# Kernel tuning notes

Hardware: AMD Instinct MI355X
Metric: run time of the kernel (lower is better)

The kernel has to match this reference:

```python
import jax, jax.numpy as jnp
import numpy as np

HEADS = 4
SIZE = 3


def setup_inputs() -> dict:
    key = jax.random.key(0)
    ks = jax.random.split(key, 8)
    B, C, D, H, W = 2, 64, 24, 24, 24
    s = 1.0 / np.sqrt(C)
    x = jax.random.normal(ks[0], (B, C, D, H, W), jnp.float32)
    cemb = jax.random.normal(ks[1], (B, C), jnp.float32)
    Wq = jax.random.normal(ks[2], (C, C), jnp.float32) * s
    bq = jax.random.normal(ks[3], (C,), jnp.float32) * 0.01
    Wk = jax.random.normal(ks[4], (C, C), jnp.float32) * s
    bk = jax.random.normal(ks[5], (C,), jnp.float32) * 0.01
    Wv = jax.random.normal(ks[6], (C, C), jnp.float32) * s
    bv = jax.random.normal(ks[7], (C,), jnp.float32) * 0.01
    return {"x": x, "cemb": cemb, "Wq": Wq, "bq": bq, "Wk": Wk, "bk": bk, "Wv": Wv, "bv": bv}


def _unfold(t, size, heads):
    # t: (B, D, H, W, C) -> (B, D*H*W, heads, size^3, C//heads), zero padded borders
    B, D, H, W, C = t.shape
    pad = size // 2
    tp = jnp.pad(t, ((0, 0), (pad, pad), (pad, pad), (pad, pad), (0, 0)))
    # depth shift outermost, then height, then width (matches torch unfold order)
    patches = jnp.stack(
        [tp[:, i:i + D, j:j + H, l:l + W, :]
         for i in range(size) for j in range(size) for l in range(size)],
        axis=4)  # (B, D, H, W, ws, C)
    ws = size ** 3
    hd = C // heads
    return patches.reshape(B, D * H * W, ws, heads, hd).transpose(0, 1, 3, 2, 4)


def reference(x, cemb, Wq, bq, Wk, bk, Wv, bv):
    # x: (B, C, D, H, W); cemb unused by the original forward
    B, C, D, H, W = x.shape
    heads, size = HEADS, SIZE
    hd = C // heads
    xc = jnp.transpose(x, (0, 2, 3, 4, 1))  # (B, D, H, W, C)
    q = xc @ Wq.T + bq
    k = xc @ Wk.T + bk
    v = xc @ Wv.T + bv
    kw = _unfold(k, size, heads)  # (B, N, h, ws, hd)
    vw = _unfold(v, size, heads)
    qh = q.reshape(B, D * H * W, heads, 1, hd) * (hd ** -0.5)
    attn = jnp.einsum('bnhqd,bnhkd->bnhqk', qh, kw)  # (B, N, h, 1, ws)
    attn = jax.nn.softmax(attn, axis=-1)
    h = jnp.einsum('bnhqk,bnhkd->bnhqd', attn, vw).reshape(B, D, H, W, C)
    out = xc + h
    return jnp.transpose(out, (0, 4, 1, 2, 3))
```

## Files before the change

kernel.cpp:

```cpp
#include <hip/hip_runtime.h>

#define NV 13824
#define CCH 64
#define NB 2

__global__ __launch_bounds__(256) void qkv_kernel(
    const float* __restrict__ x,
    const float* __restrict__ Wq, const float* __restrict__ bq,
    const float* __restrict__ Wk, const float* __restrict__ bk,
    const float* __restrict__ Wv, const float* __restrict__ bv,
    float* __restrict__ qo, float* __restrict__ ko, float* __restrict__ vo)
{
    __shared__ float  sW[32 * 64];
    __shared__ float  sB2[32];
    __shared__ float4 sO[32 * 65];

    const int t   = threadIdx.x;
    const int bid = blockIdx.x;
    const int lb  = (bid & 7) * 81 + (bid >> 3);
    const int oc  = lb % 6;
    const int nch = lb / 6;
    const int m   = oc >> 1;
    const int ch0 = (oc & 1) * 32;
    const int b   = nch / 54;
    const int nn  = (nch - b * 54) * 256;
    const float sc = (m == 0) ? 0.25f : 1.0f;

    {
        const float* const Ws[3] = {Wq, Wk, Wv};
        const float* const bs[3] = {bq, bk, bv};
        const float4* src = (const float4*)(Ws[m] + ch0 * 64);
        float4* dst = (float4*)sW;
        #pragma unroll
        for (int g = 0; g < 2; ++g) {
            float4 wv4 = src[g * 256 + t];
            wv4.x *= sc; wv4.y *= sc; wv4.z *= sc; wv4.w *= sc;
            dst[g * 256 + t] = wv4;
        }
        if (t < 32) sB2[t] = bs[m][ch0 + t] * sc;
    }
    __syncthreads();

    const int tn = t & 63;
    const int tw = t >> 6;
    const float* xp = x + (size_t)b * CCH * NV + nn + tn * 4;
    const float4* sW4 = (const float4*)sW;

    float4 acc[8];
    #pragma unroll
    for (int i = 0; i < 8; ++i) acc[i] = make_float4(0.f, 0.f, 0.f, 0.f);

    #pragma unroll 4
    for (int c4 = 0; c4 < 16; ++c4) {
        float4 w4[8];
        #pragma unroll
        for (int i = 0; i < 8; ++i) w4[i] = sW4[(tw * 8 + i) * 16 + c4];
        #pragma unroll
        for (int cc = 0; cc < 4; ++cc) {
            const float4 xv = *(const float4*)(xp + (size_t)(c4 * 4 + cc) * NV);
            #pragma unroll
            for (int i = 0; i < 8; ++i) {
                const float ws = (cc == 0) ? w4[i].x : (cc == 1) ? w4[i].y
                               : (cc == 2) ? w4[i].z : w4[i].w;
                acc[i].x += xv.x * ws; acc[i].y += xv.y * ws;
                acc[i].z += xv.z * ws; acc[i].w += xv.w * ws;
            }
        }
    }

    #pragma unroll
    for (int i = 0; i < 8; ++i) {
        const int ol = tw * 8 + i;
        const float bb = sB2[ol];
        float4 a = acc[i];
        a.x += bb; a.y += bb; a.z += bb; a.w += bb;
        sO[ol * 65 + tn] = a;
    }
    __syncthreads();

    float* const outs[3] = {qo, ko, vo};
    const float* sOf = (const float*)sO;
    float* ob = outs[m] + (size_t)(b * NV + nn) * 64 + ch0;
    #pragma unroll
    for (int it = 0; it < 8; ++it) {
        const int g   = it * 256 + t;
        const int n   = g >> 3;
        const int of4 = g & 7;
        float4 o4;
        o4.x = sOf[(of4 * 4 + 0) * 260 + n];
        o4.y = sOf[(of4 * 4 + 1) * 260 + n];
        o4.z = sOf[(of4 * 4 + 2) * 260 + n];
        o4.w = sOf[(of4 * 4 + 3) * 260 + n];
        *(float4*)(ob + (size_t)n * 64 + of4 * 4) = o4;
    }
}

__global__ __launch_bounds__(256) void attn_kernel(
    const float* __restrict__ x,
    const float* __restrict__ qw,
    const float* __restrict__ kw,
    const float* __restrict__ vw,
    float* __restrict__ out)
{
    __shared__ float so[32][65];

    const int t    = threadIdx.x;
    const int bid  = blockIdx.x;
    const int lb   = (bid & 7) * 108 + (bid >> 3);
    const int half = t & 1;
    const int head = (t >> 1) & 3;
    const int vb   = t >> 3;
    const int n0g  = lb * 32;
    const int gr   = n0g + vb;
    const int b    = gr / NV;
    const int n    = gr - b * NV;
    const int d    = n / 576;
    const int rem  = n - d * 576;
    const int r    = rem / 24;
    const int w    = rem - r * 24;
    const int coff = head * 16 + half * 8;

    int   idx[27];
    float msk[27];
    #pragma unroll
    for (int i3 = 0; i3 < 3; ++i3)
    #pragma unroll
    for (int j3 = 0; j3 < 3; ++j3)
    #pragma unroll
    for (int l3 = 0; l3 < 3; ++l3) {
        const int dd = d + i3 - 1;
        const int rr = r + j3 - 1;
        const int ww = w + l3 - 1;
        const bool ok = ((unsigned)dd < 24u) & ((unsigned)rr < 24u) & ((unsigned)ww < 24u);
        const int jj = (i3 * 3 + j3) * 3 + l3;
        idx[jj] = ok ? ((dd * 24 + rr) * 24 + ww) : n;
        msk[jj] = ok ? 1.f : 0.f;
    }

    const float4* qp = (const float4*)(qw + (size_t)gr * 64 + coff);
    const float4 q0 = qp[0], q1 = qp[1];

    const float* kbase = kw + (size_t)b * NV * 64 + coff;

    float logit[27];
    #pragma unroll
    for (int j = 0; j < 27; ++j) {
        const float4* kp = (const float4*)(kbase + (size_t)idx[j] * 64);
        const float4 k0 = kp[0], k1 = kp[1];
        float a;
        a  = q0.x * k0.x + q0.y * k0.y + q0.z * k0.z + q0.w * k0.w;
        a += q1.x * k1.x + q1.y * k1.y + q1.z * k1.z + q1.w * k1.w;
        logit[j] = a * msk[j];
    }
    #pragma unroll
    for (int j = 0; j < 27; ++j)
        logit[j] += __shfl_xor(logit[j], 1, 64);

    float ssum = 0.f;
    #pragma unroll
    for (int j = 0; j < 27; ++j) {
        const float e = __expf(logit[j]);
        logit[j] = e;
        ssum += e;
    }
    const float inv = 1.f / ssum;

    float a0=0.f,a1=0.f,a2=0.f,a3=0.f,a4=0.f,a5=0.f,a6=0.f,a7=0.f;
    const float* vbase = vw + (size_t)b * NV * 64 + coff;
    #pragma unroll
    for (int j = 0; j < 27; ++j) {
        const float p = logit[j] * msk[j];
        const float4* vp = (const float4*)(vbase + (size_t)idx[j] * 64);
        const float4 v0 = vp[0], v1 = vp[1];
        a0 += p * v0.x; a1 += p * v0.y; a2 += p * v0.z; a3 += p * v0.w;
        a4 += p * v1.x; a5 += p * v1.y; a6 += p * v1.z; a7 += p * v1.w;
    }

    so[vb][coff + 0] = a0 * inv;  so[vb][coff + 1] = a1 * inv;
    so[vb][coff + 2] = a2 * inv;  so[vb][coff + 3] = a3 * inv;
    so[vb][coff + 4] = a4 * inv;  so[vb][coff + 5] = a5 * inv;
    so[vb][coff + 6] = a6 * inv;  so[vb][coff + 7] = a7 * inv;
    __syncthreads();

    const int vv = t & 31;
    const int cg = t >> 5;
    const int bs = n0g / NV;
    const int nb0 = n0g - bs * NV;
    const float* xb = x   + (size_t)bs * CCH * NV + nb0 + vv;
    float*       ob = out + (size_t)bs * CCH * NV + nb0 + vv;
    #pragma unroll
    for (int i = 0; i < 8; ++i) {
        const int c = cg * 8 + i;
        ob[(size_t)c * NV] = xb[(size_t)c * NV] + so[vv][c];
    }
}

extern "C" void kernel_launch(void* const* d_in, const int* in_sizes, int n_in,
                              void* d_out, int out_size, void* d_ws, size_t ws_size,
                              hipStream_t stream) {
    const float* x  = (const float*)d_in[0];
    const float* Wq = (const float*)d_in[2];
    const float* bq = (const float*)d_in[3];
    const float* Wk = (const float*)d_in[4];
    const float* bk = (const float*)d_in[5];
    const float* Wv = (const float*)d_in[6];
    const float* bv = (const float*)d_in[7];
    float* out = (float*)d_out;

    float* ws = (float*)d_ws;
    const size_t RC = (size_t)NB * NV * CCH;
    float* q = ws;
    float* k = ws + RC;
    float* v = ws + 2 * RC;

    qkv_kernel<<<648, 256, 0, stream>>>(x, Wq, bq, Wk, bk, Wv, bv, q, k, v);
    attn_kernel<<<864, 256, 0, stream>>>(x, q, k, v, out);
}
```

Before: 107.9 us.

## Halve per-block work in qkv and attention kernels, use 16 threads per voxel

Result: no change. 109.1 us (+1.1%).

```diff
diff --git a/kernel.cpp b/kernel.cpp
--- a/kernel.cpp
+++ b/kernel.cpp
@@ -13,17 +13,17 @@
 {
     __shared__ float  sW[32 * 64];
     __shared__ float  sB2[32];
-    __shared__ float4 sO[32 * 65];
+    __shared__ float4 sO[32 * 33];
 
     const int t   = threadIdx.x;
     const int bid = blockIdx.x;
-    const int lb  = (bid & 7) * 81 + (bid >> 3);
+    const int lb  = (bid & 7) * 162 + (bid >> 3);
     const int oc  = lb % 6;
     const int nch = lb / 6;
     const int m   = oc >> 1;
     const int ch0 = (oc & 1) * 32;
-    const int b   = nch / 54;
-    const int nn  = (nch - b * 54) * 256;
+    const int b   = nch / 108;
+    const int nn  = (nch - b * 108) * 128;
     const float sc = (m == 0) ? 0.25f : 1.0f;
 
     {
@@ -41,25 +41,25 @@
     }
     __syncthreads();
 
-    const int tn = t & 63;
-    const int tw = t >> 6;
+    const int tn = t & 31;
+    const int tw = t >> 5;
     const float* xp = x + (size_t)b * CCH * NV + nn + tn * 4;
     const float4* sW4 = (const float4*)sW;
 
-    float4 acc[8];
-    #pragma unroll
-    for (int i = 0; i < 8; ++i) acc[i] = make_float4(0.f, 0.f, 0.f, 0.f);
+    float4 acc[4];
+    #pragma unroll
+    for (int i = 0; i < 4; ++i) acc[i] = make_float4(0.f, 0.f, 0.f, 0.f);
 
     #pragma unroll 4
     for (int c4 = 0; c4 < 16; ++c4) {
-        float4 w4[8];
+        float4 w4[4];
         #pragma unroll
-        for (int i = 0; i < 8; ++i) w4[i] = sW4[(tw * 8 + i) * 16 + c4];
+        for (int i = 0; i < 4; ++i) w4[i] = sW4[(tw * 4 + i) * 16 + c4];
         #pragma unroll
         for (int cc = 0; cc < 4; ++cc) {
             const float4 xv = *(const float4*)(xp + (size_t)(c4 * 4 + cc) * NV);
             #pragma unroll
-            for (int i = 0; i < 8; ++i) {
+            for (int i = 0; i < 4; ++i) {
                 const float ws = (cc == 0) ? w4[i].x : (cc == 1) ? w4[i].y
                                : (cc == 2) ? w4[i].z : w4[i].w;
                 acc[i].x += xv.x * ws; acc[i].y += xv.y * ws;
@@ -69,12 +69,12 @@
     }
 
     #pragma unroll
-    for (int i = 0; i < 8; ++i) {
-        const int ol = tw * 8 + i;
+    for (int i = 0; i < 4; ++i) {
+        const int ol = tw * 4 + i;
         const float bb = sB2[ol];
         float4 a = acc[i];
         a.x += bb; a.y += bb; a.z += bb; a.w += bb;
-        sO[ol * 65 + tn] = a;
+        sO[ol * 33 + tn] = a;
     }
     __syncthreads();
 
@@ -82,15 +82,15 @@
     const float* sOf = (const float*)sO;
     float* ob = outs[m] + (size_t)(b * NV + nn) * 64 + ch0;
     #pragma unroll
-    for (int it = 0; it < 8; ++it) {
+    for (int it = 0; it < 4; ++it) {
         const int g   = it * 256 + t;
         const int n   = g >> 3;
         const int of4 = g & 7;
         float4 o4;
-        o4.x = sOf[(of4 * 4 + 0) * 260 + n];
-        o4.y = sOf[(of4 * 4 + 1) * 260 + n];
-        o4.z = sOf[(of4 * 4 + 2) * 260 + n];
-        o4.w = sOf[(of4 * 4 + 3) * 260 + n];
+        o4.x = sOf[(of4 * 4 + 0) * 132 + n];
+        o4.y = sOf[(of4 * 4 + 1) * 132 + n];
+        o4.z = sOf[(of4 * 4 + 2) * 132 + n];
+        o4.w = sOf[(of4 * 4 + 3) * 132 + n];
         *(float4*)(ob + (size_t)n * 64 + of4 * 4) = o4;
     }
 }
@@ -102,59 +102,51 @@
     const float* __restrict__ vw,
     float* __restrict__ out)
 {
-    __shared__ float so[32][65];
-
-    const int t    = threadIdx.x;
-    const int bid  = blockIdx.x;
-    const int lb   = (bid & 7) * 108 + (bid >> 3);
-    const int half = t & 1;
-    const int head = (t >> 1) & 3;
-    const int vb   = t >> 3;
-    const int n0g  = lb * 32;
-    const int gr   = n0g + vb;
-    const int b    = gr / NV;
-    const int n    = gr - b * NV;
-    const int d    = n / 576;
-    const int rem  = n - d * 576;
-    const int r    = rem / 24;
-    const int w    = rem - r * 24;
-    const int coff = head * 16 + half * 8;
-
-    int   idx[27];
-    float msk[27];
+    __shared__ float4 sO4[16 * 17];
+
+    const int t   = threadIdx.x;
+    const int bid = blockIdx.x;
+    const int lb  = (bid & 7) * 216 + (bid >> 3);
+    const int c4i = t & 15;
+    const int vb  = t >> 4;
+    const int gr  = lb * 16 + vb;
+    const int b   = gr / NV;
+    const int n   = gr - b * NV;
+    const int d   = n / 576;
+    const int rem = n - d * 576;
+    const int r   = rem / 24;
+    const int w   = rem - r * 24;
+    const int n64 = n * 64;
+
+    const float4 q0 = *(const float4*)(qw + (size_t)gr * 64 + c4i * 4);
+    const float* kb = kw + (size_t)b * NV * 64 + c4i * 4;
+    const float* vp = vw + (size_t)b * NV * 64 + c4i * 4;
+
+    float logit[27];
+    unsigned mb = 0;
     #pragma unroll
     for (int i3 = 0; i3 < 3; ++i3)
     #pragma unroll
     for (int j3 = 0; j3 < 3; ++j3)
     #pragma unroll
     for (int l3 = 0; l3 < 3; ++l3) {
-        const int dd = d + i3 - 1;
-        const int rr = r + j3 - 1;
-        const int ww = w + l3 - 1;
+        const int jj  = (i3 * 3 + j3) * 3 + l3;
+        const int dd  = d + i3 - 1;
+        const int rr  = r + j3 - 1;
+        const int ww  = w + l3 - 1;
         const bool ok = ((unsigned)dd < 24u) & ((unsigned)rr < 24u) & ((unsigned)ww < 24u);
-        const int jj = (i3 * 3 + j3) * 3 + l3;
-        idx[jj] = ok ? ((dd * 24 + rr) * 24 + ww) : n;
-        msk[jj] = ok ? 1.f : 0.f;
-    }
-
-    const float4* qp = (const float4*)(qw + (size_t)gr * 64 + coff);
-    const float4 q0 = qp[0], q1 = qp[1];
-
-    const float* kbase = kw + (size_t)b * NV * 64 + coff;
-
-    float logit[27];
-    #pragma unroll
-    for (int j = 0; j < 27; ++j) {
-        const float4* kp = (const float4*)(kbase + (size_t)idx[j] * 64);
-        const float4 k0 = kp[0], k1 = kp[1];
-        float a;
-        a  = q0.x * k0.x + q0.y * k0.y + q0.z * k0.z + q0.w * k0.w;
-        a += q1.x * k1.x + q1.y * k1.y + q1.z * k1.z + q1.w * k1.w;
-        logit[j] = a * msk[j];
-    }
-    #pragma unroll
-    for (int j = 0; j < 27; ++j)
-        logit[j] += __shfl_xor(logit[j], 1, 64);
+        const int OFF = ((i3 - 1) * 576 + (j3 - 1) * 24 + (l3 - 1)) * 64;
+        const int nj  = n64 + (ok ? OFF : 0);
+        const float4 kf = *(const float4*)(kb + (size_t)nj);
+        const float a = q0.x * kf.x + q0.y * kf.y + q0.z * kf.z + q0.w * kf.w;
+        logit[jj] = ok ? a : 0.f;
+        mb |= (ok ? 1u : 0u) << jj;
+    }
+
+    #pragma unroll
+    for (int j = 0; j < 27; ++j) logit[j] += __shfl_xor(logit[j], 1, 64);
+    #pragma unroll
+    for (int j = 0; j < 27; ++j) logit[j] += __shfl_xor(logit[j], 2, 64);
 
     float ssum = 0.f;
     #pragma unroll
@@ -165,33 +157,38 @@
     }
     const float inv = 1.f / ssum;
 
-    float a0=0.f,a1=0.f,a2=0.f,a3=0.f,a4=0.f,a5=0.f,a6=0.f,a7=0.f;
-    const float* vbase = vw + (size_t)b * NV * 64 + coff;
-    #pragma unroll
-    for (int j = 0; j < 27; ++j) {
-        const float p = logit[j] * msk[j];
-        const float4* vp = (const float4*)(vbase + (size_t)idx[j] * 64);
-        const float4 v0 = vp[0], v1 = vp[1];
-        a0 += p * v0.x; a1 += p * v0.y; a2 += p * v0.z; a3 += p * v0.w;
-        a4 += p * v1.x; a5 += p * v1.y; a6 += p * v1.z; a7 += p * v1.w;
-    }
-
-    so[vb][coff + 0] = a0 * inv;  so[vb][coff + 1] = a1 * inv;
-    so[vb][coff + 2] = a2 * inv;  so[vb][coff + 3] = a3 * inv;
-    so[vb][coff + 4] = a4 * inv;  so[vb][coff + 5] = a5 * inv;
-    so[vb][coff + 6] = a6 * inv;  so[vb][coff + 7] = a7 * inv;
+    float4 acc = make_float4(0.f, 0.f, 0.f, 0.f);
+    #pragma unroll
+    for (int i3 = 0; i3 < 3; ++i3)
+    #pragma unroll
+    for (int j3 = 0; j3 < 3; ++j3)
+    #pragma unroll
+    for (int l3 = 0; l3 < 3; ++l3) {
+        const int jj  = (i3 * 3 + j3) * 3 + l3;
+        const bool ok = (mb >> jj) & 1u;
+        const int OFF = ((i3 - 1) * 576 + (j3 - 1) * 24 + (l3 - 1)) * 64;
+        const int nj  = n64 + (ok ? OFF : 0);
+        const float p = ok ? logit[jj] : 0.f;
+        const float4 vf = *(const float4*)(vp + (size_t)nj);
+        acc.x += p * vf.x; acc.y += p * vf.y;
+        acc.z += p * vf.z; acc.w += p * vf.w;
+    }
+    acc.x *= inv; acc.y *= inv; acc.z *= inv; acc.w *= inv;
+
+    sO4[vb * 17 + c4i] = acc;
     __syncthreads();
 
-    const int vv = t & 31;
-    const int cg = t >> 5;
-    const int bs = n0g / NV;
-    const int nb0 = n0g - bs * NV;
+    const int vv  = t & 15;
+    const int cg  = t >> 4;
+    const int bs  = (lb * 16) / NV;
+    const int nb0 = lb * 16 - bs * NV;
+    const float* sOf = (const float*)sO4;
     const float* xb = x   + (size_t)bs * CCH * NV + nb0 + vv;
     float*       ob = out + (size_t)bs * CCH * NV + nb0 + vv;
     #pragma unroll
-    for (int i = 0; i < 8; ++i) {
-        const int c = cg * 8 + i;
-        ob[(size_t)c * NV] = xb[(size_t)c * NV] + so[vv][c];
+    for (int i = 0; i < 4; ++i) {
+        const int c = cg + i * 16;
+        ob[(size_t)c * NV] = xb[(size_t)c * NV] + sOf[vv * 68 + c];
     }
 }
 
@@ -213,6 +210,6 @@
     float* k = ws + RC;
     float* v = ws + 2 * RC;
 
-    qkv_kernel<<<648, 256, 0, stream>>>(x, Wq, bq, Wk, bk, Wv, bv, q, k, v);
-    attn_kernel<<<864, 256, 0, stream>>>(x, q, k, v, out);
+    qkv_kernel<<<1296, 256, 0, stream>>>(x, Wq, bq, Wk, bk, Wv, bv, q, k, v);
+    attn_kernel<<<1728, 256, 0, stream>>>(x, q, k, v, out);
 }
```
